# Optimization experiments

Hardware: AMD Instinct MI355X
Metric: run time of the kernel (lower is better)

Reference implementation:

```python
import jax, jax.numpy as jnp
import numpy as np

HEAD_DIM = 64
N_HEADS = 12
ROPE_BASE = 10000.0


def _rope_tables(seq_len, head_dim, dtype=jnp.float32):
    half = head_dim // 2
    inv_freq = 1.0 / (ROPE_BASE ** (jnp.arange(0, half, dtype=jnp.float32) / half))
    pos = jnp.arange(seq_len, dtype=jnp.float32)
    freqs = pos[:, None] * inv_freq[None, :]  # (s, half)
    return jnp.cos(freqs).astype(dtype), jnp.sin(freqs).astype(dtype)


def _apply_rope(t, cos, sin):
    # t: (b, h, s, d); rotate-half convention on full head_dim (rope_fraction=1.0)
    d = t.shape[-1]
    t1, t2 = t[..., : d // 2], t[..., d // 2 :]
    cos = cos[None, None, :, :]
    sin = sin[None, None, :, :]
    return jnp.concatenate([t1 * cos - t2 * sin, t1 * sin + t2 * cos], axis=-1)


def setup_inputs() -> dict:
    key = jax.random.key(0)
    ks = jax.random.split(key, 6)
    b, s, d_model = 16, 512, 768
    x = jax.random.normal(ks[0], (b, s, d_model), dtype=jnp.float32)
    chain_ids = jax.random.randint(ks[1], (b, s), 0, 2, dtype=jnp.int32)
    attention_mask = jnp.ones((b, s), dtype=bool)
    inner = N_HEADS * HEAD_DIM
    scale = 0.02
    Wq = jax.random.normal(ks[2], (d_model, inner), dtype=jnp.float32) * scale
    Wk = jax.random.normal(ks[3], (d_model, inner), dtype=jnp.float32) * scale
    Wv = jax.random.normal(ks[4], (d_model, inner), dtype=jnp.float32) * scale
    Wo = jax.random.normal(ks[5], (inner, d_model), dtype=jnp.float32) * scale
    return {"x": x, "chain_ids": chain_ids, "attention_mask": attention_mask,
            "Wq": Wq, "Wk": Wk, "Wv": Wv, "Wo": Wo}


def reference(x, chain_ids, attention_mask, Wq, Wk, Wv, Wo):
    b, s, _ = x.shape
    h, d = N_HEADS, HEAD_DIM
    scale = d ** (-0.5)

    def proj(W):
        return jnp.einsum('bse,ef->bsf', x, W).reshape(b, s, h, d).transpose(0, 2, 1, 3)

    q = proj(Wq)  # (b, h, s, d)
    k = proj(Wk)
    v = proj(Wv)

    cos, sin = _rope_tables(s, d, x.dtype)
    q_rope = _apply_rope(q, cos, sin)
    k_rope = _apply_rope(k, cos, sin)

    scores_intra = jnp.einsum('bhsd,bhtd->bhst', q_rope, k_rope) * scale
    scores_inter = jnp.einsum('bhsd,bhtd->bhst', q, k) * scale

    # intra-chain mask (b, 1, s, s)
    intra = (chain_ids[:, None, :, None] == chain_ids[:, None, None, :])
    merged = jnp.where(intra, scores_intra, scores_inter)

    # additive padding mask (b, 1, 1, s)
    pad = jnp.where(attention_mask[:, None, None, :], 0.0, -jnp.inf).astype(x.dtype)
    merged = merged + pad

    attn = jax.nn.softmax(merged, axis=-1)
    attn = jnp.nan_to_num(attn, nan=0.0)

    out = jnp.einsum('bhst,bhtd->bhsd', attn, v)
    out = out.transpose(0, 2, 1, 3).reshape(b, s, h * d)
    return jnp.einsum('bsf,fe->bse', out, Wo)
```

## Files before the change

### kernel.cpp

```cpp
#include <hip/hip_runtime.h>
#include <stdint.h>
#include <math.h>

#define NB 16
#define NS 512
#define NH 12
#define ND 64
#define NE 768
#define NF 768

typedef __attribute__((ext_vector_type(4))) float  f32x4;
typedef __attribute__((ext_vector_type(8))) short  bf16x8;
typedef __attribute__((ext_vector_type(4))) short  bf16x4;

#define AS1(p) ((const __attribute__((address_space(1))) unsigned int*)(p))
#define AS3(p) ((__attribute__((address_space(3))) unsigned int*)(p))

__device__ __forceinline__ short f2bf(float f) {
    unsigned u = __builtin_bit_cast(unsigned, f);
    u += 0x7FFFu + ((u >> 16) & 1u);
    return (short)(u >> 16);
}
__device__ __forceinline__ float bf2f(short s) {
    unsigned u = ((unsigned)(unsigned short)s) << 16;
    return __builtin_bit_cast(float, u);
}
__device__ __forceinline__ unsigned pkbf2(float a, float b) {
    return (unsigned)(unsigned short)f2bf(a) | ((unsigned)(unsigned short)f2bf(b) << 16);
}

#define MFMA16(a, b, c) __builtin_amdgcn_mfma_f32_16x16x32_bf16((a), (b), (c), 0, 0, 0)

__device__ __forceinline__ bf16x8 lds_rd8(const short* base, int row, int cb) {
    return *(const bf16x8*)((const char*)base + (((row) * 128 + (cb)) ^ (((row) & 7) << 4)));
}

__global__ __launch_bounds__(256) void prep_kernel(float* __restrict__ cos_t,
                                                   float* __restrict__ sin_t,
                                                   const unsigned char* __restrict__ m,
                                                   int* __restrict__ flag) {
    if (blockIdx.x == 64) {
        __shared__ int any;
        if (threadIdx.x == 0) any = 0;
        __syncthreads();
        int acc = 0;
        for (int i = threadIdx.x; i < NB * NS; i += 256)
            if ((i & 3) && m[i]) acc = 1;
        if (acc) atomicOr(&any, 1);
        __syncthreads();
        if (threadIdx.x == 0) *flag = any;
        return;
    }
    int i = blockIdx.x * 256 + threadIdx.x;
    int p = i >> 5, j = i & 31;
    float inv_freq = powf(10000.0f, -(float)j / 32.0f);
    float ang = (float)p * inv_freq;
    cos_t[i] = cosf(ang);
    sin_t[i] = sinf(ang);
}

__global__ __launch_bounds__(256) void convert_x_kernel(const float* __restrict__ x,
                                                        short* __restrict__ xb) {
    int i = (blockIdx.x * 256 + threadIdx.x) * 8;
    if (i >= 8192 * 768) return;
    float4 a = *(const float4*)&x[i];
    float4 b = *(const float4*)&x[i + 4];
    bf16x8 r = { f2bf(a.x), f2bf(a.y), f2bf(a.z), f2bf(a.w),
                 f2bf(b.x), f2bf(b.y), f2bf(b.z), f2bf(b.w) };
    *(bf16x8*)&xb[i] = r;
}

__global__ __launch_bounds__(256) void convert_wt_kernel(
    const float* __restrict__ Wq, const float* __restrict__ Wk,
    const float* __restrict__ Wv, const float* __restrict__ Wo,
    short* __restrict__ Wqt, short* __restrict__ Wkt,
    short* __restrict__ Wvt, short* __restrict__ Wot) {
    const float* W  = (blockIdx.z == 0) ? Wq  : (blockIdx.z == 1) ? Wk  : (blockIdx.z == 2) ? Wv  : Wo;
    short*       Wt = (blockIdx.z == 0) ? Wqt : (blockIdx.z == 1) ? Wkt : (blockIdx.z == 2) ? Wvt : Wot;
    const int k0 = blockIdx.y * 64, n0 = blockIdx.x * 64;
    __shared__ float t[64][65];
    for (int u = threadIdx.x; u < 4096; u += 256) {
        int r = u >> 6, c = u & 63;
        t[r][c] = W[(size_t)(k0 + r) * 768 + n0 + c];
    }
    __syncthreads();
    for (int u = threadIdx.x; u < 4096; u += 256) {
        int c = u >> 6, r = u & 63;
        Wt[(size_t)(n0 + c) * 768 + k0 + r] = f2bf(t[r][c]);
    }
}

__global__ __launch_bounds__(256) void gemm_qkv_kernel(const short* __restrict__ xb,
    const short* __restrict__ Wqt, const short* __restrict__ Wkt, const short* __restrict__ Wvt,
    const float* __restrict__ cos_t, const float* __restrict__ sin_t,
    short* __restrict__ qo, short* __restrict__ ko, short* __restrict__ kpo,
    short* __restrict__ vto) {
    const int id = blockIdx.x;
    const int xcd = id & 7, rest = id >> 3;
    const int mq = rest / 18;
    const int nz = rest % 18;
    const int z  = nz / 6;
    const int n0 = (nz % 6) * 128;
    const int m0 = (xcd * 8 + mq) * 128;
    const short* Bt = (z == 0) ? Wqt : (z == 1) ? Wkt : Wvt;
    short*       O  = (z == 0) ? qo  : (z == 1) ? ko  : vto;
    __shared__ short As[128 * 64], Bs[128 * 64];
    const int tid = threadIdx.x, lane = tid & 63, wave = tid >> 6;
    const int g = lane >> 4, l15 = lane & 15;
    const int wm = wave >> 1, wn = wave & 1;
    f32x4 acc[4][4];
    #pragma unroll
    for (int i = 0; i < 4; ++i)
        #pragma unroll
        for (int j = 0; j < 4; ++j) acc[i][j] = (f32x4){0.f, 0.f, 0.f, 0.f};

    for (int kt = 0; kt < 12; ++kt) {
        __syncthreads();
        const char* Asrc = (const char*)(xb + (size_t)m0 * 768 + kt * 64);
        const char* Bsrc = (const char*)(Bt + (size_t)n0 * 768 + kt * 64);
        #pragma unroll
        for (int p = 0; p < 4; ++p) {
            int dstoff = (wave * 4 + p) * 1024;
            int off = dstoff + lane * 16;
            int row = off >> 7, slot = off & 127;
            int srcs = slot ^ ((row & 7) << 4);
            __builtin_amdgcn_global_load_lds(AS1(Asrc + (size_t)row * 1536 + srcs),
                                             AS3((char*)As + dstoff), 16, 0, 0);
            __builtin_amdgcn_global_load_lds(AS1(Bsrc + (size_t)row * 1536 + srcs),
                                             AS3((char*)Bs + dstoff), 16, 0, 0);
        }
        __syncthreads();
        __builtin_amdgcn_s_setprio(1);
        #pragma unroll
        for (int h2 = 0; h2 < 2; ++h2) {
            bf16x8 af[4], bfr[4];
            const int cb = h2 * 64 + g * 16;
            #pragma unroll
            for (int i = 0; i < 4; ++i) {
                af[i]  = lds_rd8(As, wm * 64 + i * 16 + l15, cb);
                bfr[i] = lds_rd8(Bs, wn * 64 + i * 16 + l15, cb);
            }
            #pragma unroll
            for (int i = 0; i < 4; ++i)
                #pragma unroll
                for (int j = 0; j < 4; ++j)
                    acc[i][j] = MFMA16(af[i], bfr[j], acc[i][j]);
        }
        __builtin_amdgcn_s_setprio(0);
    }
    const int hh = (n0 + wn * 64) >> 6;
    #pragma unroll
    for (int i = 0; i < 4; ++i)
        #pragma unroll
        for (int r = 0; r < 4; ++r) {
            int mm = m0 + wm * 64 + i * 16 + g * 4 + r;
            int bb = mm >> 9, ss = mm & 511;
            if (z == 2) {
                #pragma unroll
                for (int j = 0; j < 4; ++j) {
                    int dd = j * 16 + l15;
                    O[(((size_t)bb * NH + hh) * ND + dd) * NS + ss] = f2bf(acc[i][j][r]);
                }
            } else {
                size_t base = (((size_t)bb * NH + hh) * NS + ss) * ND;
                #pragma unroll
                for (int j = 0; j < 4; ++j)
                    O[base + j * 16 + l15] = f2bf(acc[i][j][r]);
                if (z == 1) {
                    #pragma unroll
                    for (int p2 = 0; p2 < 2; ++p2) {
                        int jf = p2 * 16 + l15;
                        float c = cos_t[ss * 32 + jf], s = sin_t[ss * 32 + jf];
                        float t1 = acc[i][p2][r], t2 = acc[i][p2 + 2][r];
                        kpo[base + jf]      = f2bf(t1 * c - t2 * s);
                        kpo[base + 32 + jf] = f2bf(t1 * s + t2 * c);
                    }
                }
            }
        }
}

__global__ __launch_bounds__(256) void attn_fused_kernel(
    const short* __restrict__ qr, const short* __restrict__ kr, const short* __restrict__ kp,
    const short* __restrict__ vt,
    const float* __restrict__ cos_t, const float* __restrict__ sin_t,
    const int* __restrict__ chain, const void* __restrict__ amask,
    const int* __restrict__ mflag, short* __restrict__ aout) {
    const int lid = blockIdx.x;
    const int xcd = lid & 7, idx = lid >> 3;
    const int qt = idx & 7, bhl = idx >> 3;
    const int bh = xcd * 24 + bhl;
    const int b = bh / 12, h = bh - (bh / 12) * 12;
    const int q0 = qt * 64;

    __shared__ short Kr_s[4096];
    __shared__ short Kp_s[4096];
    __shared__ short Vt_s[4096];
    __shared__ short P_s[4096];
    __shared__ int   ck_a[512];
    __shared__ float kb_a[512];

    const int tid = threadIdx.x, lane = tid & 63, wave = tid >> 6;
    const int g = lane >> 4, l15 = lane & 15;
    const int m_u8 = *mflag;
    const size_t bhNS = (size_t)bh * NS;
    const float SC = 0.18033688011f;

    for (int u = tid; u < NS; u += 256) {
        int gidx = b * NS + u;
        ck_a[u] = chain[gidx];
        int ok = m_u8 ? (int)((const unsigned char*)amask)[gidx] : ((const int*)amask)[gidx];
        kb_a[u] = ok ? 0.f : -INFINITY;
    }
    const char* qrsC = (const char*)(qr + (bhNS + q0) * ND);
    #pragma unroll
    for (int p = 0; p < 2; ++p) {
        int dstoff = (wave * 2 + p) * 1024;
        int off = dstoff + lane * 16;
        int row = off >> 7, slot = off & 127;
        int srcs = slot ^ ((row & 7) << 4);
        __builtin_amdgcn_global_load_lds(AS1(qrsC + (size_t)row * 128 + srcs),
                                         AS3((char*)Kr_s + dstoff), 16, 0, 0);
    }
    __syncthreads();
    const int qrow = wave * 16 + l15;
    bf16x8 fqr0 = lds_rd8(Kr_s, qrow, g * 16);
    bf16x8 fqr1 = lds_rd8(Kr_s, qrow, 64 + g * 16);
    bf16x8 fqp0, fqp1;
    {
        int pos = q0 + qrow;
        float4 c0 = *(const float4*)&cos_t[pos * 32 + g * 8];
        float4 c1 = *(const float4*)&cos_t[pos * 32 + g * 8 + 4];
        float4 s0 = *(const float4*)&sin_t[pos * 32 + g * 8];
        float4 s1 = *(const float4*)&sin_t[pos * 32 + g * 8 + 4];
        float cc[8] = {c0.x, c0.y, c0.z, c0.w, c1.x, c1.y, c1.z, c1.w};
        float ss[8] = {s0.x, s0.y, s0.z, s0.w, s1.x, s1.y, s1.z, s1.w};
        #pragma unroll
        for (int j = 0; j < 8; ++j) {
            float t1 = bf2f(fqr0[j]), t2 = bf2f(fqr1[j]);
            fqp0[j] = f2bf(t1 * cc[j] - t2 * ss[j]);
            fqp1[j] = f2bf(t1 * ss[j] + t2 * cc[j]);
        }
    }
    const int cqv = ck_a[q0 + qrow];

    float m_run = -INFINITY, l_run = 0.f;
    f32x4 accO[4];
    #pragma unroll
    for (int t = 0; t < 4; ++t) accO[t] = (f32x4){0.f, 0.f, 0.f, 0.f};

    const char* krC = (const char*)(kr + bhNS * ND);
    const char* kpC = (const char*)(kp + bhNS * ND);
    const char* vtC = (const char*)(vt + bhNS * ND);

    for (int kv = 0; kv < 8; ++kv) {
        const int k0s = kv * 64;
        __syncthreads();
        #pragma unroll
        for (int p = 0; p < 2; ++p) {
            int dstoff = (wave * 2 + p) * 1024;
            int off = dstoff + lane * 16;
            int row = off >> 7, slot = off & 127;
            int srcs = slot ^ ((row & 7) << 4);
            size_t koff = (size_t)(k0s + row) * 128 + srcs;
            __builtin_amdgcn_global_load_lds(AS1(krC + koff), AS3((char*)Kr_s + dstoff), 16, 0, 0);
            __builtin_amdgcn_global_load_lds(AS1(kpC + koff), AS3((char*)Kp_s + dstoff), 16, 0, 0);
            __builtin_amdgcn_global_load_lds(AS1(vtC + (size_t)row * 1024 + k0s * 2 + srcs),
                                             AS3((char*)Vt_s + dstoff), 16, 0, 0);
        }
        __syncthreads();

        float pm[4][4];
        float tm = -INFINITY;
        __builtin_amdgcn_s_setprio(1);
        #pragma unroll
        for (int t = 0; t < 4; ++t) {
            bf16x8 akr0 = lds_rd8(Kr_s, t * 16 + l15, g * 16);
            bf16x8 akr1 = lds_rd8(Kr_s, t * 16 + l15, 64 + g * 16);
            bf16x8 akp0 = lds_rd8(Kp_s, t * 16 + l15, g * 16);
            bf16x8 akp1 = lds_rd8(Kp_s, t * 16 + l15, 64 + g * 16);
            f32x4 sr = (f32x4){0.f, 0.f, 0.f, 0.f};
            f32x4 sp = (f32x4){0.f, 0.f, 0.f, 0.f};
            sr = MFMA16(akr0, fqr0, sr);
            sr = MFMA16(akr1, fqr1, sr);
            sp = MFMA16(akp0, fqp0, sp);
            sp = MFMA16(akp1, fqp1, sp);
            int4   ck4 = *(const int4*)&ck_a[k0s + t * 16 + g * 4];
            float4 kb4 = *(const float4*)&kb_a[k0s + t * 16 + g * 4];
            const int   ckk[4] = {ck4.x, ck4.y, ck4.z, ck4.w};
            const float kbb[4] = {kb4.x, kb4.y, kb4.z, kb4.w};
            #pragma unroll
            for (int r = 0; r < 4; ++r) {
                float sv = (cqv == ckk[r]) ? sp[r] : sr[r];
                sv = sv * SC + kbb[r];
                pm[t][r] = sv;
                tm = fmaxf(tm, sv);
            }
        }
        __builtin_amdgcn_s_setprio(0);

        tm = fmaxf(tm, __shfl_xor(tm, 16));
        tm = fmaxf(tm, __shfl_xor(tm, 32));
        bool skip = __all(tm - m_run <= 8.f);
        float mnew, fac;
        if (skip) { mnew = m_run; fac = 1.f; }
        else      { mnew = fmaxf(m_run, tm); fac = exp2f(m_run - mnew); }
        float psum = 0.f;
        if (mnew == -INFINITY) {
            #pragma unroll
            for (int t = 0; t < 4; ++t)
                #pragma unroll
                for (int r = 0; r < 4; ++r) pm[t][r] = 0.f;
            fac = 1.f;
        } else {
            #pragma unroll
            for (int t = 0; t < 4; ++t)
                #pragma unroll
                for (int r = 0; r < 4; ++r) {
                    float p = exp2f(pm[t][r] - mnew);
                    pm[t][r] = p;
                    psum += p;
                }
        }
        psum += __shfl_xor(psum, 16);
        psum += __shfl_xor(psum, 32);
        l_run = l_run * fac + psum;
        m_run = mnew;

        char* pwave = (char*)P_s + wave * 2048;
        int psw = (l15 & 7) << 4;
        #pragma unroll
        for (int t = 0; t < 4; ++t) {
            unsigned u0 = pkbf2(pm[t][0], pm[t][1]);
            unsigned u1 = pkbf2(pm[t][2], pm[t][3]);
            uint2 pk = {u0, u1};
            *(uint2*)(pwave + ((l15 * 128 + t * 32 + g * 8) ^ psw)) = pk;
        }
        if (!skip) {
            float f4[4];
            #pragma unroll
            for (int r = 0; r < 4; ++r) f4[r] = __shfl(fac, g * 4 + r);
            #pragma unroll
            for (int t = 0; t < 4; ++t) {
                f32x4 a = accO[t];
                a[0] *= f4[0]; a[1] *= f4[1]; a[2] *= f4[2]; a[3] *= f4[3];
                accO[t] = a;
            }
        }
        bf16x8 pa0 = *(const bf16x8*)(pwave + ((l15 * 128 + g * 16) ^ psw));
        bf16x8 pa1 = *(const bf16x8*)(pwave + ((l15 * 128 + 64 + g * 16) ^ psw));
        __builtin_amdgcn_s_setprio(1);
        #pragma unroll
        for (int dt = 0; dt < 4; ++dt) {
            bf16x8 vb0 = lds_rd8(Vt_s, dt * 16 + l15, g * 16);
            bf16x8 vb1 = lds_rd8(Vt_s, dt * 16 + l15, 64 + g * 16);
            accO[dt] = MFMA16(pa0, vb0, accO[dt]);
            accO[dt] = MFMA16(pa1, vb1, accO[dt]);
        }
        __builtin_amdgcn_s_setprio(0);
    }

    float inv[4];
    #pragma unroll
    for (int r = 0; r < 4; ++r) {
        float lv = __shfl(l_run, g * 4 + r);
        inv[r] = (lv > 0.f) ? 1.f / lv : 0.f;
    }
    #pragma unroll
    for (int dt = 0; dt < 4; ++dt)
        #pragma unroll
        for (int r = 0; r < 4; ++r) {
            int row = b * NS + q0 + wave * 16 + g * 4 + r;
            aout[(size_t)row * NF + h * ND + dt * 16 + l15] = f2bf(accO[dt][r] * inv[r]);
        }
}

__global__ __launch_bounds__(256) void gemm_out_kernel(const short* __restrict__ A,
    const short* __restrict__ Wot, float* __restrict__ out) {
    const int id = blockIdx.x;
    const int xcd = id & 7, rest = id >> 3;
    const int mq = rest / 6;
    const int n0 = (rest % 6) * 128;
    const int m0 = (xcd * 16 + mq) * 64;
    __shared__ short As[64 * 64], Bs[128 * 64];
    const int tid = threadIdx.x, lane = tid & 63, wave = tid >> 6;
    const int g = lane >> 4, l15 = lane & 15;
    const int wm = wave >> 1, wn = wave & 1;
    f32x4 acc[2][4];
    #pragma unroll
    for (int i = 0; i < 2; ++i)
        #pragma unroll
        for (int j = 0; j < 4; ++j) acc[i][j] = (f32x4){0.f, 0.f, 0.f, 0.f};

    for (int kt = 0; kt < 12; ++kt) {
        __syncthreads();
        const char* Asrc = (const char*)(A   + (size_t)m0 * 768 + kt * 64);
        const char* Bsrc = (const char*)(Wot + (size_t)n0 * 768 + kt * 64);
        #pragma unroll
        for (int p = 0; p < 2; ++p) {
            int dstoff = (wave * 2 + p) * 1024;
            int off = dstoff + lane * 16;
            int row = off >> 7, slot = off & 127;
            int srcs = slot ^ ((row & 7) << 4);
            __builtin_amdgcn_global_load_lds(AS1(Asrc + (size_t)row * 1536 + srcs),
                                             AS3((char*)As + dstoff), 16, 0, 0);
        }
        #pragma unroll
        for (int p = 0; p < 4; ++p) {
            int dstoff = (wave * 4 + p) * 1024;
            int off = dstoff + lane * 16;
            int row = off >> 7, slot = off & 127;
            int srcs = slot ^ ((row & 7) << 4);
            __builtin_amdgcn_global_load_lds(AS1(Bsrc + (size_t)row * 1536 + srcs),
                                             AS3((char*)Bs + dstoff), 16, 0, 0);
        }
        __syncthreads();
        __builtin_amdgcn_s_setprio(1);
        #pragma unroll
        for (int h2 = 0; h2 < 2; ++h2) {
            bf16x8 af[2], bfr[4];
            const int cb = h2 * 64 + g * 16;
            #pragma unroll
            for (int i = 0; i < 2; ++i)
                af[i]  = lds_rd8(As, wm * 32 + i * 16 + l15, cb);
            #pragma unroll
            for (int j = 0; j < 4; ++j)
                bfr[j] = lds_rd8(Bs, wn * 64 + j * 16 + l15, cb);
            #pragma unroll
            for (int i = 0; i < 2; ++i)
                #pragma unroll
                for (int j = 0; j < 4; ++j)
                    acc[i][j] = MFMA16(af[i], bfr[j], acc[i][j]);
        }
        __builtin_amdgcn_s_setprio(0);
    }
    #pragma unroll
    for (int i = 0; i < 2; ++i)
        #pragma unroll
        for (int r = 0; r < 4; ++r) {
            int mm = m0 + wm * 32 + i * 16 + g * 4 + r;
            #pragma unroll
            for (int j = 0; j < 4; ++j) {
                int n = n0 + wn * 64 + j * 16 + l15;
                out[(size_t)mm * NE + n] = acc[i][j][r];
            }
        }
}

extern "C" void kernel_launch(void* const* d_in, const int* in_sizes, int n_in,
                              void* d_out, int out_size, void* d_ws, size_t ws_size,
                              hipStream_t stream) {
    const float* x     = (const float*)d_in[0];
    const int*   chain = (const int*)d_in[1];
    const void*  amask = d_in[2];
    const float* Wq = (const float*)d_in[3];
    const float* Wk = (const float*)d_in[4];
    const float* Wv = (const float*)d_in[5];
    const float* Wo = (const float*)d_in[6];
    float* out = (float*)d_out;

    const size_t QSZ = (size_t)NB * NH * NS * ND;
    char* w = (char*)d_ws;
    float* cos_t = (float*)w;  w += (size_t)NS * 32 * 4;
    float* sin_t = (float*)w;  w += (size_t)NS * 32 * 4;
    int*   mflag = (int*)w;    w += 256;
    short* xb    = (short*)w;  w += (size_t)8192 * 768 * 2;
    short* Wqt   = (short*)w;  w += (size_t)768 * 768 * 2;
    short* Wkt   = (short*)w;  w += (size_t)768 * 768 * 2;
    short* Wvt   = (short*)w;  w += (size_t)768 * 768 * 2;
    short* Wot   = (short*)w;  w += (size_t)768 * 768 * 2;
    short* q_raw = (short*)w;  w += QSZ * 2;
    short* k_raw = (short*)w;  w += QSZ * 2;
    short* k_rop = (short*)w;  w += QSZ * 2;
    short* vtr   = (short*)w;  w += QSZ * 2;
    short* aout  = xb;

    prep_kernel<<<dim3(65), dim3(256), 0, stream>>>(cos_t, sin_t,
                                                    (const unsigned char*)amask, mflag);
    convert_x_kernel<<<dim3(3072), dim3(256), 0, stream>>>(x, xb);
    convert_wt_kernel<<<dim3(12, 12, 4), dim3(256), 0, stream>>>(Wq, Wk, Wv, Wo, Wqt, Wkt, Wvt, Wot);
    gemm_qkv_kernel<<<dim3(1152), dim3(256), 0, stream>>>(xb, Wqt, Wkt, Wvt, cos_t, sin_t,
                                                          q_raw, k_raw, k_rop, vtr);
    attn_fused_kernel<<<dim3(1536), dim3(256), 0, stream>>>(q_raw, k_raw, k_rop, vtr,
                                                            cos_t, sin_t, chain, amask, mflag, aout);
    gemm_out_kernel<<<dim3(768), dim3(256), 0, stream>>>(aout, Wot, out);
}
```

Measured before the change: 160.6 us.

## Fuse fp32-to-bf16 conversion of x into QKV GEMM A-tile load

Drops the separate convert_x kernel. The QKV GEMM now reads fp32 x directly, converts it to bf16 in registers and writes it into swizzled LDS, which removes one full write and read of an 8192x768 bf16 intermediate and one kernel launch. The M tile is halved to 64 and the grid doubled to 2304 blocks, raising parallelism but tripling fp32 x traffic because each row of x is re-read by 18 blocks. The A-tile load also becomes synchronous register loads instead of the async global_load_lds path.

```diff
diff --git a/kernel.cpp b/kernel.cpp
--- a/kernel.cpp
+++ b/kernel.cpp
@@ -57,17 +57,6 @@
     float ang = (float)p * inv_freq;
     cos_t[i] = cosf(ang);
     sin_t[i] = sinf(ang);
-}
-
-__global__ __launch_bounds__(256) void convert_x_kernel(const float* __restrict__ x,
-                                                        short* __restrict__ xb) {
-    int i = (blockIdx.x * 256 + threadIdx.x) * 8;
-    if (i >= 8192 * 768) return;
-    float4 a = *(const float4*)&x[i];
-    float4 b = *(const float4*)&x[i + 4];
-    bf16x8 r = { f2bf(a.x), f2bf(a.y), f2bf(a.z), f2bf(a.w),
-                 f2bf(b.x), f2bf(b.y), f2bf(b.z), f2bf(b.w) };
-    *(bf16x8*)&xb[i] = r;
 }
 
 __global__ __launch_bounds__(256) void convert_wt_kernel(
@@ -90,7 +79,7 @@
     }
 }
 
-__global__ __launch_bounds__(256) void gemm_qkv_kernel(const short* __restrict__ xb,
+__global__ __launch_bounds__(256) void gemm_qkv_kernel(const float* __restrict__ x,
     const short* __restrict__ Wqt, const short* __restrict__ Wkt, const short* __restrict__ Wvt,
     const float* __restrict__ cos_t, const float* __restrict__ sin_t,
     short* __restrict__ qo, short* __restrict__ ko, short* __restrict__ kpo,
@@ -101,31 +90,41 @@
     const int nz = rest % 18;
     const int z  = nz / 6;
     const int n0 = (nz % 6) * 128;
-    const int m0 = (xcd * 8 + mq) * 128;
+    const int m0 = (xcd * 16 + mq) * 64;
     const short* Bt = (z == 0) ? Wqt : (z == 1) ? Wkt : Wvt;
     short*       O  = (z == 0) ? qo  : (z == 1) ? ko  : vto;
-    __shared__ short As[128 * 64], Bs[128 * 64];
+    __shared__ short As[64 * 64], Bs[128 * 64];
     const int tid = threadIdx.x, lane = tid & 63, wave = tid >> 6;
     const int g = lane >> 4, l15 = lane & 15;
     const int wm = wave >> 1, wn = wave & 1;
-    f32x4 acc[4][4];
-    #pragma unroll
-    for (int i = 0; i < 4; ++i)
+    const int arow = tid >> 4, ac4 = (tid & 15) * 4;
+    f32x4 acc[2][4];
+    #pragma unroll
+    for (int i = 0; i < 2; ++i)
         #pragma unroll
         for (int j = 0; j < 4; ++j) acc[i][j] = (f32x4){0.f, 0.f, 0.f, 0.f};
 
     for (int kt = 0; kt < 12; ++kt) {
-        __syncthreads();
-        const char* Asrc = (const char*)(xb + (size_t)m0 * 768 + kt * 64);
-        const char* Bsrc = (const char*)(Bt + (size_t)n0 * 768 + kt * 64);
+        const int k0 = kt * 64;
+        float4 av[4];
+        #pragma unroll
+        for (int p = 0; p < 4; ++p)
+            av[p] = *(const float4*)&x[(size_t)(m0 + arow + 16 * p) * 768 + k0 + ac4];
+        const char* Bsrc = (const char*)(Bt + (size_t)n0 * 768 + k0);
+        __syncthreads();
+        #pragma unroll
+        for (int p = 0; p < 4; ++p) {
+            int row = arow + 16 * p;
+            int byteo = (row * 128 + ac4 * 2) ^ ((row & 7) << 4);
+            uint2 w0 = { pkbf2(av[p].x, av[p].y), pkbf2(av[p].z, av[p].w) };
+            *(uint2*)((char*)As + byteo) = w0;
+        }
         #pragma unroll
         for (int p = 0; p < 4; ++p) {
             int dstoff = (wave * 4 + p) * 1024;
             int off = dstoff + lane * 16;
             int row = off >> 7, slot = off & 127;
             int srcs = slot ^ ((row & 7) << 4);
-            __builtin_amdgcn_global_load_lds(AS1(Asrc + (size_t)row * 1536 + srcs),
-                                             AS3((char*)As + dstoff), 16, 0, 0);
             __builtin_amdgcn_global_load_lds(AS1(Bsrc + (size_t)row * 1536 + srcs),
                                              AS3((char*)Bs + dstoff), 16, 0, 0);
         }
@@ -133,15 +132,16 @@
         __builtin_amdgcn_s_setprio(1);
         #pragma unroll
         for (int h2 = 0; h2 < 2; ++h2) {
-            bf16x8 af[4], bfr[4];
+            bf16x8 af[2], bfr[4];
             const int cb = h2 * 64 + g * 16;
             #pragma unroll
-            for (int i = 0; i < 4; ++i) {
-                af[i]  = lds_rd8(As, wm * 64 + i * 16 + l15, cb);
-                bfr[i] = lds_rd8(Bs, wn * 64 + i * 16 + l15, cb);
-            }
-            #pragma unroll
-            for (int i = 0; i < 4; ++i)
+            for (int i = 0; i < 2; ++i)
+                af[i]  = lds_rd8(As, wm * 32 + i * 16 + l15, cb);
+            #pragma unroll
+            for (int j = 0; j < 4; ++j)
+                bfr[j] = lds_rd8(Bs, wn * 64 + j * 16 + l15, cb);
+            #pragma unroll
+            for (int i = 0; i < 2; ++i)
                 #pragma unroll
                 for (int j = 0; j < 4; ++j)
                     acc[i][j] = MFMA16(af[i], bfr[j], acc[i][j]);
@@ -150,10 +150,10 @@
     }
     const int hh = (n0 + wn * 64) >> 6;
     #pragma unroll
-    for (int i = 0; i < 4; ++i)
+    for (int i = 0; i < 2; ++i)
         #pragma unroll
         for (int r = 0; r < 4; ++r) {
-            int mm = m0 + wm * 64 + i * 16 + g * 4 + r;
+            int mm = m0 + wm * 32 + i * 16 + g * 4 + r;
             int bb = mm >> 9, ss = mm & 511;
             if (z == 2) {
                 #pragma unroll
@@ -464,7 +464,7 @@
     float* cos_t = (float*)w;  w += (size_t)NS * 32 * 4;
     float* sin_t = (float*)w;  w += (size_t)NS * 32 * 4;
     int*   mflag = (int*)w;    w += 256;
-    short* xb    = (short*)w;  w += (size_t)8192 * 768 * 2;
+    short* aout  = (short*)w;  w += (size_t)8192 * 768 * 2;
     short* Wqt   = (short*)w;  w += (size_t)768 * 768 * 2;
     short* Wkt   = (short*)w;  w += (size_t)768 * 768 * 2;
     short* Wvt   = (short*)w;  w += (size_t)768 * 768 * 2;
@@ -473,13 +473,11 @@
     short* k_raw = (short*)w;  w += QSZ * 2;
     short* k_rop = (short*)w;  w += QSZ * 2;
     short* vtr   = (short*)w;  w += QSZ * 2;
-    short* aout  = xb;
 
     prep_kernel<<<dim3(65), dim3(256), 0, stream>>>(cos_t, sin_t,
                                                     (const unsigned char*)amask, mflag);
-    convert_x_kernel<<<dim3(3072), dim3(256), 0, stream>>>(x, xb);
     convert_wt_kernel<<<dim3(12, 12, 4), dim3(256), 0, stream>>>(Wq, Wk, Wv, Wo, Wqt, Wkt, Wvt, Wot);
-    gemm_qkv_kernel<<<dim3(1152), dim3(256), 0, stream>>>(xb, Wqt, Wkt, Wvt, cos_t, sin_t,
+    gemm_qkv_kernel<<<dim3(2304), dim3(256), 0, stream>>>(x, Wqt, Wkt, Wvt, cos_t, sin_t,
                                                           q_raw, k_raw, k_rop, vtr);
     attn_fused_kernel<<<dim3(1536), dim3(256), 0, stream>>>(q_raw, k_raw, k_rop, vtr,
                                                             cos_t, sin_t, chain, amask, mflag, aout);
```

Result: faster. 157.0 us (-2.3%).

## Double-buffer LDS in QKV and output GEMMs and halve QKV M-tile

Applied to the files above, without the earlier changes.

Both GEMM kernels now use two LDS buffers, issuing the global-to-LDS loads for the next K tile before computing on the current one, with a single waitcnt and barrier per iteration. The QKV GEMM tile shrinks from 128x128 to 64x128, which doubles the grid to 2304 blocks and halves per-thread accumulators. The aim is to hide global load latency behind MFMA work and raise occupancy and wave count. The cost is more LDS per block and more redundant reads of the weight tiles across the extra M blocks.

```diff
diff --git a/kernel.cpp b/kernel.cpp
--- a/kernel.cpp
+++ b/kernel.cpp
@@ -101,59 +101,81 @@
     const int nz = rest % 18;
     const int z  = nz / 6;
     const int n0 = (nz % 6) * 128;
-    const int m0 = (xcd * 8 + mq) * 128;
+    const int m0 = (xcd * 16 + mq) * 64;
     const short* Bt = (z == 0) ? Wqt : (z == 1) ? Wkt : Wvt;
     short*       O  = (z == 0) ? qo  : (z == 1) ? ko  : vto;
-    __shared__ short As[128 * 64], Bs[128 * 64];
+    __shared__ short As[2][64 * 64], Bs[2][128 * 64];
     const int tid = threadIdx.x, lane = tid & 63, wave = tid >> 6;
     const int g = lane >> 4, l15 = lane & 15;
     const int wm = wave >> 1, wn = wave & 1;
-    f32x4 acc[4][4];
-    #pragma unroll
-    for (int i = 0; i < 4; ++i)
+    f32x4 acc[2][4];
+    #pragma unroll
+    for (int i = 0; i < 2; ++i)
         #pragma unroll
         for (int j = 0; j < 4; ++j) acc[i][j] = (f32x4){0.f, 0.f, 0.f, 0.f};
 
-    for (int kt = 0; kt < 12; ++kt) {
-        __syncthreads();
+    auto STAGE = [&](short* Ad, short* Bd, int kt) {
         const char* Asrc = (const char*)(xb + (size_t)m0 * 768 + kt * 64);
         const char* Bsrc = (const char*)(Bt + (size_t)n0 * 768 + kt * 64);
+        #pragma unroll
+        for (int p = 0; p < 2; ++p) {
+            int dstoff = (wave * 2 + p) * 1024;
+            int off = dstoff + lane * 16;
+            int row = off >> 7, slot = off & 127;
+            int srcs = slot ^ ((row & 7) << 4);
+            __builtin_amdgcn_global_load_lds(AS1(Asrc + (size_t)row * 1536 + srcs),
+                                             AS3((char*)Ad + dstoff), 16, 0, 0);
+        }
         #pragma unroll
         for (int p = 0; p < 4; ++p) {
             int dstoff = (wave * 4 + p) * 1024;
             int off = dstoff + lane * 16;
             int row = off >> 7, slot = off & 127;
             int srcs = slot ^ ((row & 7) << 4);
-            __builtin_amdgcn_global_load_lds(AS1(Asrc + (size_t)row * 1536 + srcs),
-                                             AS3((char*)As + dstoff), 16, 0, 0);
             __builtin_amdgcn_global_load_lds(AS1(Bsrc + (size_t)row * 1536 + srcs),
-                                             AS3((char*)Bs + dstoff), 16, 0, 0);
-        }
-        __syncthreads();
+                                             AS3((char*)Bd + dstoff), 16, 0, 0);
+        }
+    };
+    auto COMPUTE = [&](const short* Asb, const short* Bsb) {
         __builtin_amdgcn_s_setprio(1);
         #pragma unroll
         for (int h2 = 0; h2 < 2; ++h2) {
-            bf16x8 af[4], bfr[4];
+            bf16x8 af[2], bfr[4];
             const int cb = h2 * 64 + g * 16;
             #pragma unroll
-            for (int i = 0; i < 4; ++i) {
-                af[i]  = lds_rd8(As, wm * 64 + i * 16 + l15, cb);
-                bfr[i] = lds_rd8(Bs, wn * 64 + i * 16 + l15, cb);
-            }
-            #pragma unroll
-            for (int i = 0; i < 4; ++i)
+            for (int i = 0; i < 2; ++i)
+                af[i]  = lds_rd8(Asb, wm * 32 + i * 16 + l15, cb);
+            #pragma unroll
+            for (int j = 0; j < 4; ++j)
+                bfr[j] = lds_rd8(Bsb, wn * 64 + j * 16 + l15, cb);
+            #pragma unroll
+            for (int i = 0; i < 2; ++i)
                 #pragma unroll
                 for (int j = 0; j < 4; ++j)
                     acc[i][j] = MFMA16(af[i], bfr[j], acc[i][j]);
         }
         __builtin_amdgcn_s_setprio(0);
-    }
+    };
+
+    STAGE(As[0], Bs[0], 0);
+    asm volatile("s_waitcnt vmcnt(0)" ::: "memory");
+    __builtin_amdgcn_s_barrier();
+    int cur = 0;
+    for (int kt = 0; kt < 11; ++kt) {
+        STAGE(As[cur ^ 1], Bs[cur ^ 1], kt + 1);
+        COMPUTE(As[cur], Bs[cur]);
+        asm volatile("s_waitcnt vmcnt(0)" ::: "memory");
+        __builtin_amdgcn_s_barrier();
+        cur ^= 1;
+    }
+    COMPUTE(As[cur], Bs[cur]);
+
     const int hh = (n0 + wn * 64) >> 6;
     #pragma unroll
-    for (int i = 0; i < 4; ++i)
+    for (int i = 0; i < 2; ++i)
         #pragma unroll
         for (int r = 0; r < 4; ++r) {
-            int mm = m0 + wm * 64 + i * 16 + g * 4 + r;
+            int mm = m0 + wm * 32 + i * 16 + g * 4 + r;
             int bb = mm >> 9, ss = mm & 511;
             if (z == 2) {
                 #pragma unroll
@@ -382,7 +404,7 @@
     const int mq = rest / 6;
     const int n0 = (rest % 6) * 128;
     const int m0 = (xcd * 16 + mq) * 64;
-    __shared__ short As[64 * 64], Bs[128 * 64];
+    __shared__ short As[2][64 * 64], Bs[2][128 * 64];
     const int tid = threadIdx.x, lane = tid & 63, wave = tid >> 6;
     const int g = lane >> 4, l15 = lane & 15;
     const int wm = wave >> 1, wn = wave & 1;
@@ -392,8 +414,7 @@
         #pragma unroll
         for (int j = 0; j < 4; ++j) acc[i][j] = (f32x4){0.f, 0.f, 0.f, 0.f};
 
-    for (int kt = 0; kt < 12; ++kt) {
-        __syncthreads();
+    auto STAGE = [&](short* Ad, short* Bd, int kt) {
         const char* Asrc = (const char*)(A   + (size_t)m0 * 768 + kt * 64);
         const char* Bsrc = (const char*)(Wot + (size_t)n0 * 768 + kt * 64);
         #pragma unroll
@@ -403,7 +424,7 @@
             int row = off >> 7, slot = off & 127;
             int srcs = slot ^ ((row & 7) << 4);
             __builtin_amdgcn_global_load_lds(AS1(Asrc + (size_t)row * 1536 + srcs),
-                                             AS3((char*)As + dstoff), 16, 0, 0);
+                                             AS3((char*)Ad + dstoff), 16, 0, 0);
         }
         #pragma unroll
         for (int p = 0; p < 4; ++p) {
@@ -412,9 +433,10 @@
             int row = off >> 7, slot = off & 127;
             int srcs = slot ^ ((row & 7) << 4);
             __builtin_amdgcn_global_load_lds(AS1(Bsrc + (size_t)row * 1536 + srcs),
-                                             AS3((char*)Bs + dstoff), 16, 0, 0);
-        }
-        __syncthreads();
+                                             AS3((char*)Bd + dstoff), 16, 0, 0);
+        }
+    };
+    auto COMPUTE = [&](const short* Asb, const short* Bsb) {
         __builtin_amdgcn_s_setprio(1);
         #pragma unroll
         for (int h2 = 0; h2 < 2; ++h2) {
@@ -422,10 +444,10 @@
             const int cb = h2 * 64 + g * 16;
             #pragma unroll
             for (int i = 0; i < 2; ++i)
-                af[i]  = lds_rd8(As, wm * 32 + i * 16 + l15, cb);
+                af[i]  = lds_rd8(Asb, wm * 32 + i * 16 + l15, cb);
             #pragma unroll
             for (int j = 0; j < 4; ++j)
-                bfr[j] = lds_rd8(Bs, wn * 64 + j * 16 + l15, cb);
+                bfr[j] = lds_rd8(Bsb, wn * 64 + j * 16 + l15, cb);
             #pragma unroll
             for (int i = 0; i < 2; ++i)
                 #pragma unroll
@@ -433,7 +455,21 @@
                     acc[i][j] = MFMA16(af[i], bfr[j], acc[i][j]);
         }
         __builtin_amdgcn_s_setprio(0);
-    }
+    };
+
+    STAGE(As[0], Bs[0], 0);
+    asm volatile("s_waitcnt vmcnt(0)" ::: "memory");
+    __builtin_amdgcn_s_barrier();
+    int cur = 0;
+    for (int kt = 0; kt < 11; ++kt) {
+        STAGE(As[cur ^ 1], Bs[cur ^ 1], kt + 1);
+        COMPUTE(As[cur], Bs[cur]);
+        asm volatile("s_waitcnt vmcnt(0)" ::: "memory");
+        __builtin_amdgcn_s_barrier();
+        cur ^= 1;
+    }
+    COMPUTE(As[cur], Bs[cur]);
+
     #pragma unroll
     for (int i = 0; i < 2; ++i)
         #pragma unroll
@@ -479,7 +515,7 @@
                                                     (const unsigned char*)amask, mflag);
     convert_x_kernel<<<dim3(3072), dim3(256), 0, stream>>>(x, xb);
     convert_wt_kernel<<<dim3(12, 12, 4), dim3(256), 0, stream>>>(Wq, Wk, Wv, Wo, Wqt, Wkt, Wvt, Wot);
-    gemm_qkv_kernel<<<dim3(1152), dim3(256), 0, stream>>>(xb, Wqt, Wkt, Wvt, cos_t, sin_t,
+    gemm_qkv_kernel<<<dim3(2304), dim3(256), 0, stream>>>(xb, Wqt, Wkt, Wvt, cos_t, sin_t,
                                                           q_raw, k_raw, k_rop, vtr);
     attn_fused_kernel<<<dim3(1536), dim3(256), 0, stream>>>(q_raw, k_raw, k_rop, vtr,
                                                             cos_t, sin_t, chain, amask, mflag, aout);
```

New measurement: 157.2 us. 2.1% less time.
